# Performance work log

Hardware: AMD Instinct MI355X
Metric: run time of the kernel (lower is better)

Reference implementation:

```python
import jax, jax.numpy as jnp
import numpy as np

BN_EPS = 1e-5

def _knn_chunked(xt, k, chunk):
    # xt: [B, N, D]; returns idx [B, N, k] of nearest neighbors (self excluded)
    B, N, D = xt.shape
    sq = jnp.sum(xt * xt, axis=-1)  # [B, N]
    parts = []
    for s in range(0, N, chunk):
        e = min(N, s + chunk)
        xq = xt[:, s:e, :]  # [B, q, D]
        # squared pairwise distance, chunked over query rows
        dist = sq[:, s:e, None] + sq[:, None, :] - 2.0 * jnp.einsum('bqd,bnd->bqn', xq, xt)
        rows = jnp.arange(s, e)
        self_mask = (jnp.arange(N)[None, :] == rows[:, None])  # [q, N]
        dist = jnp.where(self_mask[None, :, :], jnp.inf, dist)
        _, idx = jax.lax.top_k(-dist, k)  # smallest distances
        parts.append(idx)
    return jnp.concatenate(parts, axis=1)  # [B, N, k]

def setup_inputs() -> dict:
    key = jax.random.key(0)
    k1, k2 = jax.random.split(key)
    B, C, N = 4, 64, 8192
    c_out = 64
    x = jax.random.normal(k1, (B, C, N), dtype=jnp.float32)
    W = jax.random.normal(k2, (c_out, 2 * C), dtype=jnp.float32) * (1.0 / np.sqrt(2 * C))
    gamma = jnp.ones((c_out,), dtype=jnp.float32)
    beta = jnp.zeros((c_out,), dtype=jnp.float32)
    return {"x": x, "W": W, "gamma": gamma, "beta": beta, "k": 20, "knn_chunk_size": 1024}

def reference(x, W, gamma, beta, k, knn_chunk_size):
    # x: [B, C, N]
    B, C, N = x.shape
    xt = jnp.transpose(x, (0, 2, 1))  # [B, N, C]
    idx = jax.lax.stop_gradient(_knn_chunked(xt, k, knn_chunk_size))  # [B, N, k]
    neigh = jax.vmap(lambda pts, ind: pts[ind])(xt, idx)  # [B, N, k, C]
    center = xt[:, :, None, :]  # [B, N, 1, C]
    edge = jnp.concatenate([neigh - center, jnp.broadcast_to(center, neigh.shape)], axis=-1)  # [B,N,k,2C]
    h = jnp.einsum('bnkc,oc->bnko', edge, W)  # 1x1 conv
    # BatchNorm2d in training mode: stats over (B, N, k) per output channel, biased var
    mean = jnp.mean(h, axis=(0, 1, 2))
    var = jnp.mean(jnp.square(h - mean), axis=(0, 1, 2))
    h = (h - mean) * jax.lax.rsqrt(var + BN_EPS) * gamma + beta
    h = jax.nn.relu(h)
    out = jnp.max(h, axis=2)  # max over neighbors -> [B, N, c_out]
    return jnp.transpose(out, (0, 2, 1))  # [B, c_out, N]
```

## Files before the change

kernel.cpp:

```cpp
#include <hip/hip_runtime.h>

typedef _Float16 half8 __attribute__((ext_vector_type(8)));
typedef float f32x4 __attribute__((ext_vector_type(4)));

#define B_ 4
#define C_ 64
#define N_ 8192
#define K_ 20
#define LCELL 8
#define NSPLIT 4
#define NCAND (16 * LCELL * NSPLIT)
#define CNT_TOTAL (B_ * N_ * K_)
#define BN_EPSF 1e-5f

__device__ __forceinline__ f32x4 max4(f32x4 a, f32x4 b) {
  f32x4 r;
  r.x = fmaxf(a.x, b.x); r.y = fmaxf(a.y, b.y);
  r.z = fmaxf(a.z, b.z); r.w = fmaxf(a.w, b.w);
  return r;
}
__device__ __forceinline__ f32x4 min4(f32x4 a, f32x4 b) {
  f32x4 r;
  r.x = fminf(a.x, b.x); r.y = fminf(a.y, b.y);
  r.z = fminf(a.z, b.z); r.w = fminf(a.w, b.w);
  return r;
}

__global__ __launch_bounds__(256) void prep_kernel(
    const float* __restrict__ x, const float* __restrict__ W,
    float* __restrict__ xt, _Float16* __restrict__ xt16,
    float* __restrict__ sq, double* __restrict__ sqd,
    float* __restrict__ y1, float* __restrict__ y2) {
  __shared__ float xs[64 * 68];
  int b = blockIdx.x >> 7;
  int n0 = (blockIdx.x & 127) * 64;
  int t = threadIdx.x;
  int lane = t & 63;
  int wv = t >> 6;
#pragma unroll
  for (int i = 0; i < 16; ++i) {
    int lin = i * 256 + t;
    int c = lin >> 6, j = lin & 63;
    xs[j * 68 + c] = x[((b * 64 + c) * N_) + n0 + j];
  }
  float4 w1[16], w2[16];
  const float4* wr = (const float4*)(W + lane * 128);
#pragma unroll
  for (int u = 0; u < 16; ++u) {
    w1[u] = wr[u];
    w2[u] = wr[16 + u];
  }
  __syncthreads();
#pragma unroll 2
  for (int i = 0; i < 16; ++i) {
    int nl = i * 4 + wv;
    const float4* xr = (const float4*)&xs[nl * 68];
    float d1 = 0.f, d2 = 0.f;
#pragma unroll
    for (int u = 0; u < 16; ++u) {
      float4 xv = xr[u];
      d1 = fmaf(xv.x, w1[u].x, d1); d1 = fmaf(xv.y, w1[u].y, d1);
      d1 = fmaf(xv.z, w1[u].z, d1); d1 = fmaf(xv.w, w1[u].w, d1);
      d2 = fmaf(xv.x, w2[u].x, d2); d2 = fmaf(xv.y, w2[u].y, d2);
      d2 = fmaf(xv.z, w2[u].z, d2); d2 = fmaf(xv.w, w2[u].w, d2);
    }
    int n = n0 + nl;
    y1[((b * N_) + n) * 64 + lane] = d1;
    y2[((b * N_) + n) * 64 + lane] = d2 - d1;
  }
#pragma unroll
  for (int i = 0; i < 16; ++i) {
    int lin = i * 256 + t;
    int c = lin & 63, nl = lin >> 6;
    float v = xs[nl * 68 + c];
    size_t o = ((size_t)(b * N_) + n0 + nl) * 64 + c;
    xt[o] = v;
    xt16[o] = (_Float16)v;
  }
  if (t < 64) {
    float s = 0.f;
    double sd = 0.0;
#pragma unroll
    for (int c = 0; c < 64; ++c) {
      float v = xs[t * 68 + c];
      s = fmaf(v, v, s);
      sd = fma((double)v, (double)v, sd);
    }
    sq[b * N_ + n0 + t] = s + 512.0f;
    sqd[b * N_ + n0 + t] = sd;
  }
}

__global__ __launch_bounds__(256, 4) void knn_mfma_kernel(
    const _Float16* __restrict__ xt16, const float* __restrict__ sq,
    int* __restrict__ pidx) {
  __shared__ alignas(16) char bufB[2][9216];
  __shared__ float bufS[2][64];
  int t = threadIdx.x;
  int wave = t >> 6;
  int lane = t & 63;
  int col = lane & 15;
  int quad = lane >> 4;
  int blk = blockIdx.x;
  int split = blk & 3;
  int qt = (blk >> 2) & 127;
  int b = blk >> 9;
  int q0 = qt * 64 + wave * 16;
  size_t bbase = (size_t)b * N_;

  const _Float16* arow = xt16 + (bbase + q0 + col) * 64;
  half8 A0 = *(const half8*)(arow + quad * 8);
  half8 A1 = *(const half8*)(arow + 32 + quad * 8);

  int dl[4][LCELL];
#pragma unroll
  for (int r = 0; r < 4; ++r)
#pragma unroll
    for (int j = 0; j < LCELL; ++j) dl[r][j] = 0x7fffffff;

#define PAIR_INSERT(accX, accY, sA, sB, CTB)                                 \
  {                                                                          \
    const int ctb_ = (CTB);                                                  \
    _Pragma("unroll") for (int r = 0; r < 4; ++r) {                          \
      float kA = fmaf((accX)[r], -2.0f, (sA));                               \
      float kB = fmaf((accY)[r], -2.0f, (sB));                               \
      int va = (__float_as_int(kA) & ~255) | ctb_;                           \
      int vb = (__float_as_int(kB) & ~255) | (ctb_ + 1);                     \
      int lo = min(va, vb), hi = max(va, vb);                                \
      int o0 = min(dl[r][0], lo);                                            \
      int o1 = min(min(dl[r][1], max(dl[r][0], lo)), hi);                    \
      int o2 = min(min(dl[r][2], max(dl[r][1], lo)), max(dl[r][0], hi));     \
      int o3 = min(min(dl[r][3], max(dl[r][2], lo)), max(dl[r][1], hi));     \
      int o4 = min(min(dl[r][4], max(dl[r][3], lo)), max(dl[r][2], hi));     \
      int o5 = min(min(dl[r][5], max(dl[r][4], lo)), max(dl[r][3], hi));     \
      int o6 = min(min(dl[r][6], max(dl[r][5], lo)), max(dl[r][4], hi));     \
      int o7 = min(min(dl[r][7], max(dl[r][6], lo)), max(dl[r][5], hi));     \
      dl[r][0] = o0; dl[r][1] = o1; dl[r][2] = o2; dl[r][3] = o3;            \
      dl[r][4] = o4; dl[r][5] = o5; dl[r][6] = o6; dl[r][7] = o7;            \
    }                                                                        \
  }

  int c0 = split * (N_ / NSPLIT);
  const _Float16* gpanel = xt16 + (bbase + c0) * 64;
  const float* spanel = sq + bbase + c0;

  int r0 = lane >> 3, e0 = lane & 7;

  int4 rA0, rA1, rB0, rB1;
  float sA = 0.f, sB = 0.f;

#define LOADR(Ra, Rb, Sv, CH)                                              \
  {                                                                        \
    const _Float16* gt = gpanel + ((size_t)(CH)*64 + wave * 16) * 64;      \
    Ra = *(const int4*)(gt + lane * 8);                                    \
    Rb = *(const int4*)(gt + 512 + lane * 8);                              \
    Sv = spanel[(CH)*64 + wave * 16 + col];                                \
  }
#define WRITEB(BUF, Ra, Rb, Sv)                                            \
  {                                                                        \
    char* lt = &bufB[BUF][wave * 2304];                                    \
    *(int4*)(lt + r0 * 144 + e0 * 16) = Ra;                                \
    *(int4*)(lt + (r0 + 8) * 144 + e0 * 16) = Rb;                          \
    if (lane < 16) bufS[BUF][wave * 16 + lane] = Sv;                       \
  }
#define CONSUME(BUF, CH)                                                   \
  {                                                                        \
    const char* lb = bufB[BUF];                                            \
    const float* sb = bufS[BUF];                                           \
    const f32x4 z = {0.f, 0.f, 0.f, 0.f};                                  \
    half8 F0 = *(const half8*)(lb + 0 * 2304 + col * 144 + quad * 16);     \
    half8 F1 = *(const half8*)(lb + 0 * 2304 + col * 144 + (4 + quad) * 16); \
    half8 G0 = *(const half8*)(lb + 1 * 2304 + col * 144 + quad * 16);     \
    half8 G1 = *(const half8*)(lb + 1 * 2304 + col * 144 + (4 + quad) * 16); \
    f32x4 a0 = __builtin_amdgcn_mfma_f32_16x16x32_f16(A0, F0, z, 0, 0, 0); \
    a0 = __builtin_amdgcn_mfma_f32_16x16x32_f16(A1, F1, a0, 0, 0, 0);      \
    f32x4 a1 = __builtin_amdgcn_mfma_f32_16x16x32_f16(A0, G0, z, 0, 0, 0); \
    a1 = __builtin_amdgcn_mfma_f32_16x16x32_f16(A1, G1, a1, 0, 0, 0);      \
    half8 H0 = *(const half8*)(lb + 2 * 2304 + col * 144 + quad * 16);     \
    half8 H1 = *(const half8*)(lb + 2 * 2304 + col * 144 + (4 + quad) * 16); \
    half8 I0 = *(const half8*)(lb + 3 * 2304 + col * 144 + quad * 16);     \
    half8 I1 = *(const half8*)(lb + 3 * 2304 + col * 144 + (4 + quad) * 16); \
    f32x4 a2 = __builtin_amdgcn_mfma_f32_16x16x32_f16(A0, H0, z, 0, 0, 0); \
    a2 = __builtin_amdgcn_mfma_f32_16x16x32_f16(A1, H1, a2, 0, 0, 0);      \
    f32x4 a3 = __builtin_amdgcn_mfma_f32_16x16x32_f16(A0, I0, z, 0, 0, 0); \
    a3 = __builtin_amdgcn_mfma_f32_16x16x32_f16(A1, I1, a3, 0, 0, 0);      \
    float s0 = sb[col], s1 = sb[16 + col];                                 \
    float s2 = sb[32 + col], s3 = sb[48 + col];                            \
    PAIR_INSERT(a0, a1, s0, s1, (CH)*4);                                   \
    PAIR_INSERT(a2, a3, s2, s3, (CH)*4 + 2);                               \
  }

  LOADR(rA0, rA1, sA, 0);
  LOADR(rB0, rB1, sB, 1);
  WRITEB(0, rA0, rA1, sA);
  __syncthreads();

  for (int ch = 0; ch < 32; ch += 2) {
    if (ch + 2 < 32) LOADR(rA0, rA1, sA, ch + 2);
    WRITEB(1, rB0, rB1, sB);
    CONSUME(0, ch);
    __syncthreads();
    if (ch + 3 < 32) LOADR(rB0, rB1, sB, ch + 3);
    if (ch + 2 < 32) WRITEB(0, rA0, rA1, sA);
    CONSUME(1, ch + 1);
    __syncthreads();
  }
#undef PAIR_INSERT
#undef LOADR
#undef WRITEB
#undef CONSUME

#pragma unroll
  for (int r = 0; r < 4; ++r) {
    int q = q0 + quad * 4 + r;
    int* o = pidx + (bbase + q) * NCAND + split * (16 * LCELL) + col * LCELL;
#pragma unroll
    for (int j = 0; j < LCELL; ++j) o[j] = dl[r][j];
  }
}

__global__ __launch_bounds__(256) void refine_kernel(
    const float* __restrict__ xt, const double* __restrict__ sqd,
    const int* __restrict__ pidx, int* __restrict__ idxf) {
  __shared__ float qs[4][64];
  __shared__ int slds[4][32];
  __shared__ double klds[4][32];
  int tid = threadIdx.x;
  int wave = tid >> 6, lane = tid & 63;
  int p = blockIdx.x * 4 + wave;
  int b = p >> 13;
  size_t bbase = (size_t)b * N_;
  int plocal = p & (N_ - 1);

  if (lane < 16) {
    ((f32x4*)qs[wave])[lane] = ((const f32x4*)(xt + (size_t)p * 64))[lane];
  }
  const int* pi = pidx + (size_t)p * NCAND + lane * 8;
  int4 ca = *(const int4*)pi;
  int4 cb = *(const int4*)(pi + 4);
  int colsplit = (lane & 15) + (lane >> 4) * (N_ / NSPLIT);
  int v0 = ca.x, v1 = ca.y, v2 = ca.z, v3 = ca.w;
  int v4 = cb.x, v5 = cb.y, v6 = cb.z, v7 = cb.w;
  if ((((v0 & 255) << 4) + colsplit) == plocal) v0 = 0x7fffffff;
  if ((((v1 & 255) << 4) + colsplit) == plocal) v1 = 0x7fffffff;
  if ((((v2 & 255) << 4) + colsplit) == plocal) v2 = 0x7fffffff;
  if ((((v3 & 255) << 4) + colsplit) == plocal) v3 = 0x7fffffff;
  if ((((v4 & 255) << 4) + colsplit) == plocal) v4 = 0x7fffffff;
  if ((((v5 & 255) << 4) + colsplit) == plocal) v5 = 0x7fffffff;
  if ((((v6 & 255) << 4) + colsplit) == plocal) v6 = 0x7fffffff;
  if ((((v7 & 255) << 4) + colsplit) == plocal) v7 = 0x7fffffff;
  {
    int lo, hi;
    lo = min(v0, v1); hi = max(v0, v1); v0 = lo; v1 = hi;
    lo = min(v1, v2); hi = max(v1, v2); v1 = lo; v2 = hi;
    lo = min(v2, v3); hi = max(v2, v3); v2 = lo; v3 = hi;
    lo = min(v3, v4); hi = max(v3, v4); v3 = lo; v4 = hi;
    lo = min(v4, v5); hi = max(v4, v5); v4 = lo; v5 = hi;
    lo = min(v5, v6); hi = max(v5, v6); v5 = lo; v6 = hi;
    lo = min(v6, v7); hi = max(v6, v7); v6 = lo; v7 = hi;
  }
  int vh = v0, h1 = v1, h2 = v2, h3 = v3, h4 = v4, h5 = v5, h6 = v6,
      h7 = v7;

  unsigned long long mylt = (1ull << lane) - 1;
  int* sl = slds[wave];
#pragma unroll
  for (int s = 0; s < 32; ++s) {
    int m = vh;
    m = min(m, __shfl_xor(m, 1, 64));
    m = min(m, __shfl_xor(m, 2, 64));
    m = min(m, __shfl_xor(m, 4, 64));
    m = min(m, __shfl_xor(m, 8, 64));
    m = min(m, __shfl_xor(m, 16, 64));
    m = min(m, __shfl_xor(m, 32, 64));
    bool eq = (vh == m);
    unsigned long long bal = __ballot(eq);
    if (eq && ((bal & mylt) == 0)) {
      sl[s] = ((vh & 255) << 4) + colsplit;
      vh = h1; h1 = h2; h2 = h3; h3 = h4; h4 = h5; h5 = h6; h6 = h7;
      h7 = 0x7fffffff;
    }
  }

  int ci = sl[lane & 31];
  int half = lane >> 5;
  const f32x4* cr = (const f32x4*)(xt + (bbase + ci) * 64) + half * 8;
  const f32x4* qr = (const f32x4*)qs[wave] + half * 8;
  double a0 = 0.0, a1 = 0.0, a2 = 0.0, a3 = 0.0;
#pragma unroll
  for (int t2 = 0; t2 < 8; ++t2) {
    f32x4 cv = cr[t2];
    f32x4 qv = qr[t2];
    a0 = fma((double)cv.x, (double)qv.x, a0);
    a1 = fma((double)cv.y, (double)qv.y, a1);
    a2 = fma((double)cv.z, (double)qv.z, a2);
    a3 = fma((double)cv.w, (double)qv.w, a3);
  }
  double dot = (a0 + a1) + (a2 + a3);
  dot += __shfl_xor(dot, 32, 64);
  double kv = 1e300;
  if (lane < 32) {
    double kd = fma(dot, -2.0, sqd[bbase + ci]) + 1024.0;
    kv = __longlong_as_double(
        (__double_as_longlong(kd) & ~0x1FFFLL) | (long long)ci);
    klds[wave][lane] = kv;
  }

  if (lane < 32) {
    const double* kl = klds[wave];
    int c0 = 0, c1 = 0, c2 = 0, c3 = 0;
#pragma unroll
    for (int t2 = 0; t2 < 32; t2 += 4) {
      c0 += (kl[t2] < kv) ? 1 : 0;
      c1 += (kl[t2 + 1] < kv) ? 1 : 0;
      c2 += (kl[t2 + 2] < kv) ? 1 : 0;
      c3 += (kl[t2 + 3] < kv) ? 1 : 0;
    }
    int rank = (c0 + c1) + (c2 + c3);
    if (rank < K_) idxf[(size_t)p * K_ + rank] = ci;
  }
}

__global__ __launch_bounds__(256) void stats_kernel(
    const float* __restrict__ y1, const float* __restrict__ y2,
    const int* __restrict__ idxf, float* __restrict__ maxh,
    float* __restrict__ minh, float* __restrict__ gsum,
    float* __restrict__ gsq) {
  __shared__ float lsum[64], lsq[64];
  int tid = threadIdx.x;
  if (tid < 64) { lsum[tid] = 0.f; lsq[tid] = 0.f; }
  __syncthreads();
  int wv = tid >> 6, lane = tid & 63;
  int u = lane & 15, jb = lane >> 4;
  int p0 = blockIdx.x * 16 + wv * 4;
  size_t nb = (size_t)((p0 >> 13) * N_);
  f32x4 css = {0.f, 0.f, 0.f, 0.f}, cqq = {0.f, 0.f, 0.f, 0.f};
#pragma unroll
  for (int it = 0; it < 4; ++it) {
    int p = p0 + it;
    int idxval = (lane < K_) ? idxf[(size_t)p * K_ + lane] : 0;
    int n0 = __shfl(idxval, jb, 64);
    int n1 = __shfl(idxval, jb + 4, 64);
    int n2 = __shfl(idxval, jb + 8, 64);
    int n3 = __shfl(idxval, jb + 12, 64);
    int n4 = __shfl(idxval, jb + 16, 64);
    f32x4 g0 = ((const f32x4*)(y1 + (nb + n0) * 64))[u];
    f32x4 g1 = ((const f32x4*)(y1 + (nb + n1) * 64))[u];
    f32x4 g2 = ((const f32x4*)(y1 + (nb + n2) * 64))[u];
    f32x4 g3 = ((const f32x4*)(y1 + (nb + n3) * 64))[u];
    f32x4 g4 = ((const f32x4*)(y1 + (nb + n4) * 64))[u];
    f32x4 mx = g0, mn = g0, sm = g0, s2 = g0 * g0;
    mx = max4(mx, g1); mn = min4(mn, g1); sm += g1; s2 += g1 * g1;
    mx = max4(mx, g2); mn = min4(mn, g2); sm += g2; s2 += g2 * g2;
    mx = max4(mx, g3); mn = min4(mn, g3); sm += g3; s2 += g3 * g3;
    mx = max4(mx, g4); mn = min4(mn, g4); sm += g4; s2 += g4 * g4;
#pragma unroll
    for (int c = 0; c < 4; ++c) {
      mx[c] = fmaxf(mx[c], __shfl_xor(mx[c], 16, 64));
      mx[c] = fmaxf(mx[c], __shfl_xor(mx[c], 32, 64));
      mn[c] = fminf(mn[c], __shfl_xor(mn[c], 16, 64));
      mn[c] = fminf(mn[c], __shfl_xor(mn[c], 32, 64));
      sm[c] += __shfl_xor(sm[c], 16, 64);
      sm[c] += __shfl_xor(sm[c], 32, 64);
      s2[c] += __shfl_xor(s2[c], 16, 64);
      s2[c] += __shfl_xor(s2[c], 32, 64);
    }
    if (jb == 0) {
      f32x4 y2c = ((const f32x4*)(y2 + (size_t)p * 64))[u];
      ((f32x4*)(maxh + (size_t)p * 64))[u] = mx + y2c;
      ((f32x4*)(minh + (size_t)p * 64))[u] = mn + y2c;
      css += sm + 20.0f * y2c;
      cqq += s2 + 2.0f * y2c * sm + 20.0f * y2c * y2c;
    }
  }
  if (jb == 0) {
#pragma unroll
    for (int c = 0; c < 4; ++c) {
      atomicAdd(&lsum[u * 4 + c], css[c]);
      atomicAdd(&lsq[u * 4 + c], cqq[c]);
    }
  }
  __syncthreads();
  if (tid < 64) {
    atomicAdd(&gsum[tid], lsum[tid]);
    atomicAdd(&gsq[tid], lsq[tid]);
  }
}

__global__ __launch_bounds__(256) void final_kernel(
    const float* __restrict__ maxh, const float* __restrict__ minh,
    const float* __restrict__ gsum, const float* __restrict__ gsq,
    const float* __restrict__ gamma, const float* __restrict__ beta,
    float* __restrict__ out) {
  __shared__ float sc[64], cc_[64];
  __shared__ float tile[64 * 65];
  int b = blockIdx.x >> 7;
  int n0 = (blockIdx.x & 127) * 64;
  int t = threadIdx.x;
  if (t < 64) {
    float mean = gsum[t] * (1.0f / CNT_TOTAL);
    float var = gsq[t] * (1.0f / CNT_TOTAL) - mean * mean;
    float s = gamma[t] * rsqrtf(var + BN_EPSF);
    sc[t] = s;
    cc_[t] = beta[t] - mean * s;
  }
  __syncthreads();
#pragma unroll
  for (int i = 0; i < 16; ++i) {
    int lin = i * 256 + t;
    int o = lin & 63, nl = lin >> 6;
    size_t off = ((size_t)(b * N_) + n0 + nl) * 64 + o;
    float s = sc[o];
    float v = (s >= 0.f) ? maxh[off] : minh[off];
    float val = fmaxf(fmaf(v, s, cc_[o]), 0.f);
    tile[o * 65 + nl] = val;
  }
  __syncthreads();
#pragma unroll
  for (int i = 0; i < 16; ++i) {
    int lin = i * 256 + t;
    int nl = lin & 63, o = lin >> 6;
    out[((size_t)(b * 64) + o) * N_ + n0 + nl] = tile[o * 65 + nl];
  }
}

extern "C" void kernel_launch(void* const* d_in, const int* in_sizes, int n_in,
                              void* d_out, int out_size, void* d_ws,
                              size_t ws_size, hipStream_t stream) {
  const float* x = (const float*)d_in[0];
  const float* W = (const float*)d_in[1];
  const float* gamma = (const float*)d_in[2];
  const float* beta = (const float*)d_in[3];
  float* out = (float*)d_out;

  char* ws = (char*)d_ws;
  size_t off = 0;
  auto alloc = [&](size_t bytes) {
    char* p = ws + off;
    off += (bytes + 255) & ~(size_t)255;
    return p;
  };
  float* xt = (float*)alloc((size_t)B_ * N_ * 64 * 4);
  _Float16* xt16 = (_Float16*)alloc((size_t)B_ * N_ * 64 * 2);
  float* y1 = (float*)alloc((size_t)B_ * N_ * 64 * 4);
  float* y2 = (float*)alloc((size_t)B_ * N_ * 64 * 4);
  float* sq = (float*)alloc((size_t)B_ * N_ * 4);
  double* sqd = (double*)alloc((size_t)B_ * N_ * 8);
  int* pidx = (int*)alloc((size_t)B_ * N_ * NCAND * 4);
  float* maxh = (float*)alloc((size_t)B_ * N_ * 64 * 4);
  int* idxf = (int*)alloc((size_t)B_ * N_ * K_ * 4);
  float* gsum = (float*)alloc(256);
  float* gsq = (float*)alloc(256);
  float* minh = (float*)pidx;

  hipMemsetAsync(gsum, 0, 256, stream);
  hipMemsetAsync(gsq, 0, 256, stream);

  prep_kernel<<<B_ * (N_ / 64), 256, 0, stream>>>(x, W, xt, xt16, sq, sqd,
                                                  y1, y2);
  knn_mfma_kernel<<<B_ * (N_ / 64) * NSPLIT, 256, 0, stream>>>(xt16, sq, pidx);
  refine_kernel<<<(B_ * N_) / 4, 256, 0, stream>>>(xt, sqd, pidx, idxf);
  stats_kernel<<<(B_ * N_) / 16, 256, 0, stream>>>(y1, y2, idxf, maxh, minh,
                                                   gsum, gsq);
  final_kernel<<<B_ * (N_ / 64), 256, 0, stream>>>(maxh, minh, gsum, gsq,
                                                   gamma, beta, out);
}
```

Measured before the change: 378.5 us.

## Process two query points per wavefront in kNN refine kernel

Each wavefront in the refine kernel now handles two query points instead of one. The 32-step wave-wide min selection interleaves the shuffle reductions for both points, which gives more instruction-level parallelism and amortises the reduction loop. In the distance stage each half-wave computes a full 64-dim dot product for its own point, so no cross-half shuffle is needed and all 64 lanes do ranking work instead of 32. The cost is more registers and LDS per wave and half as many blocks.

New measurement: 373.2 us. Within noise of the previous version (-1.4%).

```diff
diff --git a/kernel.cpp b/kernel.cpp
--- a/kernel.cpp
+++ b/kernel.cpp
@@ -222,73 +222,91 @@
 __global__ __launch_bounds__(256) void refine_kernel(
     const float* __restrict__ xt, const double* __restrict__ sqd,
     const int* __restrict__ pidx, int* __restrict__ idxf) {
-  __shared__ float qs[4][64];
-  __shared__ int slds[4][32];
-  __shared__ double klds[4][32];
+  __shared__ float qs[4][2][64];
+  __shared__ int slds[4][2][32];
+  __shared__ double klds[4][2][32];
   int tid = threadIdx.x;
   int wave = tid >> 6, lane = tid & 63;
-  int p = blockIdx.x * 4 + wave;
-  int b = p >> 13;
+  int pA = blockIdx.x * 8 + wave * 2;
+  int pB = pA + 1;
+  int b = pA >> 13;
   size_t bbase = (size_t)b * N_;
-  int plocal = p & (N_ - 1);
+  int plA = pA & (N_ - 1), plB = pB & (N_ - 1);
 
   if (lane < 16) {
-    ((f32x4*)qs[wave])[lane] = ((const f32x4*)(xt + (size_t)p * 64))[lane];
-  }
-  const int* pi = pidx + (size_t)p * NCAND + lane * 8;
-  int4 ca = *(const int4*)pi;
-  int4 cb = *(const int4*)(pi + 4);
+    ((f32x4*)qs[wave][0])[lane] = ((const f32x4*)(xt + (size_t)pA * 64))[lane];
+  } else if (lane < 32) {
+    int l = lane - 16;
+    ((f32x4*)qs[wave][1])[l] = ((const f32x4*)(xt + (size_t)pB * 64))[l];
+  }
+
+  const int* piA = pidx + (size_t)pA * NCAND + lane * 8;
+  const int* piB = pidx + (size_t)pB * NCAND + lane * 8;
+  int4 ca0 = *(const int4*)piA;
+  int4 ca1 = *(const int4*)(piA + 4);
+  int4 cb0 = *(const int4*)piB;
+  int4 cb1 = *(const int4*)(piB + 4);
   int colsplit = (lane & 15) + (lane >> 4) * (N_ / NSPLIT);
-  int v0 = ca.x, v1 = ca.y, v2 = ca.z, v3 = ca.w;
-  int v4 = cb.x, v5 = cb.y, v6 = cb.z, v7 = cb.w;
-  if ((((v0 & 255) << 4) + colsplit) == plocal) v0 = 0x7fffffff;
-  if ((((v1 & 255) << 4) + colsplit) == plocal) v1 = 0x7fffffff;
-  if ((((v2 & 255) << 4) + colsplit) == plocal) v2 = 0x7fffffff;
-  if ((((v3 & 255) << 4) + colsplit) == plocal) v3 = 0x7fffffff;
-  if ((((v4 & 255) << 4) + colsplit) == plocal) v4 = 0x7fffffff;
-  if ((((v5 & 255) << 4) + colsplit) == plocal) v5 = 0x7fffffff;
-  if ((((v6 & 255) << 4) + colsplit) == plocal) v6 = 0x7fffffff;
-  if ((((v7 & 255) << 4) + colsplit) == plocal) v7 = 0x7fffffff;
-  {
-    int lo, hi;
-    lo = min(v0, v1); hi = max(v0, v1); v0 = lo; v1 = hi;
-    lo = min(v1, v2); hi = max(v1, v2); v1 = lo; v2 = hi;
-    lo = min(v2, v3); hi = max(v2, v3); v2 = lo; v3 = hi;
-    lo = min(v3, v4); hi = max(v3, v4); v3 = lo; v4 = hi;
-    lo = min(v4, v5); hi = max(v4, v5); v4 = lo; v5 = hi;
-    lo = min(v5, v6); hi = max(v5, v6); v5 = lo; v6 = hi;
-    lo = min(v6, v7); hi = max(v6, v7); v6 = lo; v7 = hi;
-  }
-  int vh = v0, h1 = v1, h2 = v2, h3 = v3, h4 = v4, h5 = v5, h6 = v6,
-      h7 = v7;
+
+  int uA0 = ca0.x, uA1 = ca0.y, uA2 = ca0.z, uA3 = ca0.w;
+  int uA4 = ca1.x, uA5 = ca1.y, uA6 = ca1.z, uA7 = ca1.w;
+  int uB0 = cb0.x, uB1 = cb0.y, uB2 = cb0.z, uB3 = cb0.w;
+  int uB4 = cb1.x, uB5 = cb1.y, uB6 = cb1.z, uB7 = cb1.w;
+#define EXCL(v, pl) if (((((v)&255) << 4) + colsplit) == (pl)) (v) = 0x7fffffff;
+  EXCL(uA0, plA) EXCL(uA1, plA) EXCL(uA2, plA) EXCL(uA3, plA)
+  EXCL(uA4, plA) EXCL(uA5, plA) EXCL(uA6, plA) EXCL(uA7, plA)
+  EXCL(uB0, plB) EXCL(uB1, plB) EXCL(uB2, plB) EXCL(uB3, plB)
+  EXCL(uB4, plB) EXCL(uB5, plB) EXCL(uB6, plB) EXCL(uB7, plB)
+#undef EXCL
+#define BUB(a, b_) { int lo_ = min(a, b_), hi_ = max(a, b_); a = lo_; b_ = hi_; }
+  BUB(uA0, uA1) BUB(uA1, uA2) BUB(uA2, uA3) BUB(uA3, uA4)
+  BUB(uA4, uA5) BUB(uA5, uA6) BUB(uA6, uA7)
+  BUB(uB0, uB1) BUB(uB1, uB2) BUB(uB2, uB3) BUB(uB3, uB4)
+  BUB(uB4, uB5) BUB(uB5, uB6) BUB(uB6, uB7)
+#undef BUB
 
   unsigned long long mylt = (1ull << lane) - 1;
-  int* sl = slds[wave];
+  int* slA = slds[wave][0];
+  int* slB = slds[wave][1];
 #pragma unroll
   for (int s = 0; s < 32; ++s) {
-    int m = vh;
-    m = min(m, __shfl_xor(m, 1, 64));
-    m = min(m, __shfl_xor(m, 2, 64));
-    m = min(m, __shfl_xor(m, 4, 64));
-    m = min(m, __shfl_xor(m, 8, 64));
-    m = min(m, __shfl_xor(m, 16, 64));
-    m = min(m, __shfl_xor(m, 32, 64));
-    bool eq = (vh == m);
-    unsigned long long bal = __ballot(eq);
-    if (eq && ((bal & mylt) == 0)) {
-      sl[s] = ((vh & 255) << 4) + colsplit;
-      vh = h1; h1 = h2; h2 = h3; h3 = h4; h4 = h5; h5 = h6; h6 = h7;
-      h7 = 0x7fffffff;
-    }
-  }
-
-  int ci = sl[lane & 31];
+    int mA = uA0, mB = uB0;
+    mA = min(mA, __shfl_xor(mA, 1, 64));
+    mB = min(mB, __shfl_xor(mB, 1, 64));
+    mA = min(mA, __shfl_xor(mA, 2, 64));
+    mB = min(mB, __shfl_xor(mB, 2, 64));
+    mA = min(mA, __shfl_xor(mA, 4, 64));
+    mB = min(mB, __shfl_xor(mB, 4, 64));
+    mA = min(mA, __shfl_xor(mA, 8, 64));
+    mB = min(mB, __shfl_xor(mB, 8, 64));
+    mA = min(mA, __shfl_xor(mA, 16, 64));
+    mB = min(mB, __shfl_xor(mB, 16, 64));
+    mA = min(mA, __shfl_xor(mA, 32, 64));
+    mB = min(mB, __shfl_xor(mB, 32, 64));
+    bool eqA = (uA0 == mA);
+    bool eqB = (uB0 == mB);
+    unsigned long long balA = __ballot(eqA);
+    unsigned long long balB = __ballot(eqB);
+    if (eqA && ((balA & mylt) == 0)) {
+      slA[s] = ((uA0 & 255) << 4) + colsplit;
+      uA0 = uA1; uA1 = uA2; uA2 = uA3; uA3 = uA4; uA4 = uA5; uA5 = uA6;
+      uA6 = uA7; uA7 = 0x7fffffff;
+    }
+    if (eqB && ((balB & mylt) == 0)) {
+      slB[s] = ((uB0 & 255) << 4) + colsplit;
+      uB0 = uB1; uB1 = uB2; uB2 = uB3; uB3 = uB4; uB4 = uB5; uB5 = uB6;
+      uB6 = uB7; uB7 = 0x7fffffff;
+    }
+  }
+
   int half = lane >> 5;
-  const f32x4* cr = (const f32x4*)(xt + (bbase + ci) * 64) + half * 8;
-  const f32x4* qr = (const f32x4*)qs[wave] + half * 8;
+  int s32 = lane & 31;
+  int ci = slds[wave][half][s32];
+  const f32x4* cr = (const f32x4*)(xt + (bbase + ci) * 64);
+  const f32x4* qr = (const f32x4*)qs[wave][half];
   double a0 = 0.0, a1 = 0.0, a2 = 0.0, a3 = 0.0;
 #pragma unroll
-  for (int t2 = 0; t2 < 8; ++t2) {
+  for (int t2 = 0; t2 < 16; ++t2) {
     f32x4 cv = cr[t2];
     f32x4 qv = qr[t2];
     a0 = fma((double)cv.x, (double)qv.x, a0);
@@ -297,17 +315,13 @@
     a3 = fma((double)cv.w, (double)qv.w, a3);
   }
   double dot = (a0 + a1) + (a2 + a3);
-  dot += __shfl_xor(dot, 32, 64);
-  double kv = 1e300;
-  if (lane < 32) {
-    double kd = fma(dot, -2.0, sqd[bbase + ci]) + 1024.0;
-    kv = __longlong_as_double(
-        (__double_as_longlong(kd) & ~0x1FFFLL) | (long long)ci);
-    klds[wave][lane] = kv;
-  }
-
-  if (lane < 32) {
-    const double* kl = klds[wave];
+  double kd = fma(dot, -2.0, sqd[bbase + ci]) + 1024.0;
+  double kv = __longlong_as_double(
+      (__double_as_longlong(kd) & ~0x1FFFLL) | (long long)ci);
+  klds[wave][half][s32] = kv;
+
+  {
+    const double* kl = klds[wave][half];
     int c0 = 0, c1 = 0, c2 = 0, c3 = 0;
 #pragma unroll
     for (int t2 = 0; t2 < 32; t2 += 4) {
@@ -317,7 +331,8 @@
       c3 += (kl[t2 + 3] < kv) ? 1 : 0;
     }
     int rank = (c0 + c1) + (c2 + c3);
-    if (rank < K_) idxf[(size_t)p * K_ + rank] = ci;
+    int pdst = half ? pB : pA;
+    if (rank < K_) idxf[(size_t)pdst * K_ + rank] = ci;
   }
 }
 
@@ -459,7 +474,7 @@
   prep_kernel<<<B_ * (N_ / 64), 256, 0, stream>>>(x, W, xt, xt16, sq, sqd,
                                                   y1, y2);
   knn_mfma_kernel<<<B_ * (N_ / 64) * NSPLIT, 256, 0, stream>>>(xt16, sq, pidx);
-  refine_kernel<<<(B_ * N_) / 4, 256, 0, stream>>>(xt, sqd, pidx, idxf);
+  refine_kernel<<<(B_ * N_) / 8, 256, 0, stream>>>(xt, sqd, pidx, idxf);
   stats_kernel<<<(B_ * N_) / 16, 256, 0, stream>>>(y1, y2, idxf, maxh, minh,
                                                    gsum, gsq);
   final_kernel<<<B_ * (N_ / 64), 256, 0, stream>>>(maxh, minh, gsum, gsq,
```
